# Kernel tuning notes

Hardware: AMD Instinct MI355X
Metric: run time of the kernel (lower is better)

## Reference

```python
import jax, jax.numpy as jnp
import numpy as np

N, E, B = 16000, 256000, 64
H = 4
DIMS = [960, 512, 256, 128]  # per-layer input dims; output dim of layer i is DIMS[i+1] = HID[i]*H
HID = [128, 64, 32]


def setup_inputs() -> dict:
    key = jax.random.key(0)
    ks = jax.random.split(key, 16)
    inp = {}
    inp["x"] = jax.random.normal(ks[0], (N, DIMS[0]), jnp.float32)
    inp["edge_index"] = jax.random.randint(ks[1], (2, E), 0, N)
    inp["batch"] = jnp.sort(jax.random.randint(ks[2], (N,), 0, B))
    k = 3
    for i in range(3):
        din, c = DIMS[i], HID[i]
        s = 1.0 / np.sqrt(din).astype(np.float32)
        inp[f"Wl{i+1}"] = jax.random.normal(ks[k], (din, H * c), jnp.float32) * s; k += 1
        inp[f"Wr{i+1}"] = jax.random.normal(ks[k], (din, H * c), jnp.float32) * s; k += 1
        inp[f"att{i+1}"] = jax.random.normal(ks[k], (H, c), jnp.float32) * (1.0 / np.sqrt(c).astype(np.float32)); k += 1
        inp[f"b{i+1}"] = jnp.zeros((H * c,), jnp.float32)
        inp[f"gnw{i+1}"] = jnp.ones((H * c,), jnp.float32)
        inp[f"gnb{i+1}"] = jnp.zeros((H * c,), jnp.float32)
        inp[f"gnm{i+1}"] = jnp.ones((H * c,), jnp.float32)
    d = DIMS[-1]
    inp["aW1"] = jax.random.normal(ks[k], (d, 128), jnp.float32) * (1.0 / np.sqrt(d).astype(np.float32)); k += 1
    inp["ab1"] = jnp.zeros((128,), jnp.float32)
    inp["aW2"] = jax.random.normal(ks[k], (128, 1), jnp.float32) * (1.0 / np.sqrt(128).astype(np.float32)); k += 1
    inp["ab2"] = jnp.zeros((1,), jnp.float32)
    return inp


def _gatv2(x, src, dst, Wl, Wr, att, bias):
    # PyG GATv2Conv, concat=True, negative_slope=0.2 (self-loops already in src/dst)
    n = x.shape[0]
    h, c = att.shape
    xl = (x @ Wl).reshape(n, h, c)
    xr = (x @ Wr).reshape(n, h, c)
    e = jax.nn.leaky_relu(xl[src] + xr[dst], negative_slope=0.2)  # [E,H,C]
    logit = jnp.einsum('ehc,hc->eh', e, att)                      # [E,H]
    m = jax.ops.segment_max(logit, dst, num_segments=n)
    m = jnp.nan_to_num(m, neginf=0.0)
    p = jnp.exp(logit - m[dst])
    z = jax.ops.segment_sum(p, dst, num_segments=n)
    alpha = p / (z[dst] + 1e-16)                                  # segment softmax over dst
    out = jax.ops.segment_sum(alpha[:, :, None] * xl[src], dst, num_segments=n)
    return out.reshape(n, h * c) + bias


def _graphnorm(x, w, b, ms, eps=1e-5):
    # PyG GraphNorm with batch=None: normalize over all nodes as one graph
    mean = jnp.mean(x, axis=0, keepdims=True)
    xc = x - ms * mean
    var = jnp.mean(xc * xc, axis=0, keepdims=True)
    return w * xc / jnp.sqrt(var + eps) + b


def reference(x, edge_index, batch,
              Wl1, Wr1, att1, b1, gnw1, gnb1, gnm1,
              Wl2, Wr2, att2, b2, gnw2, gnb2, gnm2,
              Wl3, Wr3, att3, b3, gnw3, gnb3, gnm3,
              aW1, ab1, aW2, ab2):
    n = x.shape[0]
    loop = jnp.arange(n)
    src = jnp.concatenate([edge_index[0], loop])  # add self-loops (PyG default)
    dst = jnp.concatenate([edge_index[1], loop])
    layers = [(Wl1, Wr1, att1, b1, gnw1, gnb1, gnm1),
              (Wl2, Wr2, att2, b2, gnw2, gnb2, gnm2),
              (Wl3, Wr3, att3, b3, gnw3, gnb3, gnm3)]
    for Wl, Wr, att, bb, gw, gb, gm in layers:
        x = _gatv2(x, src, dst, Wl, Wr, att, bb)
        x = _graphnorm(x, gw, gb, gm)
        x = jax.nn.relu(x)
    # AttentionalAggregation pooling: gate MLP -> segment softmax over graphs -> weighted sum
    gate = jax.nn.relu(x @ aW1 + ab1) @ aW2 + ab2  # [N,1]
    mg = jax.ops.segment_max(gate, batch, num_segments=B)
    mg = jnp.nan_to_num(mg, neginf=0.0)
    pg = jnp.exp(gate - mg[batch])
    zg = jax.ops.segment_sum(pg, batch, num_segments=B)
    a = pg / (zg[batch] + 1e-16)
    return jax.ops.segment_sum(a * x, batch, num_segments=B)  # [B, 128]
```

## Files before the change

kernel.cpp:

```cpp
#include <hip/hip_runtime.h>
#include <cstdint>
#include <cstddef>
#include <math.h>


typedef _Float16  h16x8  __attribute__((ext_vector_type(8)));
typedef _Float16  h16x4  __attribute__((ext_vector_type(4)));
typedef _Float16  h16x2  __attribute__((ext_vector_type(2)));
typedef float     f32x4  __attribute__((ext_vector_type(4)));

template<int R> struct HV;
template<> struct HV<8> { using T = h16x8; };
template<> struct HV<4> { using T = h16x4; };
template<> struct HV<2> { using T = h16x2; };

__device__ __forceinline__ void gload_lds16(const void* g, void* l) {
    __builtin_amdgcn_global_load_lds(
        (const __attribute__((address_space(1))) uint32_t*)g,
        (__attribute__((address_space(3))) uint32_t*)l, 16, 0, 0);
}

__device__ __forceinline__ int swz_k(int k, int row) {
    return (k & ~31) | ((((k >> 3) & 3) ^ ((row >> 1) & 3)) << 3) | (k & 7);
}

__device__ __forceinline__ void gn_coef(float s1, float s2, float w, float b,
                                        float ms, float invN, float& al, float& be) {
    float mean = s1 * invN;
    float ex2  = s2 * invN;
    float a    = ms * mean;
    float var  = ex2 - 2.f * a * mean + a * a;
    al = w * rsqrtf(var + 1e-5f);
    be = b - a * al;
}

__device__ __forceinline__ void conv_elem(int t, const float* __restrict__ Wl,
                                          const float* __restrict__ Wr,
                                          _Float16* __restrict__ Wt, int K, int HC) {
    int k = t / HC, n = t - k * HC;
    const int ks = swz_k(k, n);
    Wt[(size_t)n * K + ks] = (_Float16)Wl[t];
    if (Wr) Wt[(size_t)(HC + n) * K + ks] = (_Float16)Wr[t];
}

__global__ __launch_bounds__(256) void conv_all(
        const float* __restrict__ Wl0, const float* __restrict__ Wr0, _Float16* __restrict__ T0,
        const float* __restrict__ Wl1, const float* __restrict__ Wr1, _Float16* __restrict__ T1,
        const float* __restrict__ Wl2, const float* __restrict__ Wr2, _Float16* __restrict__ T2,
        const float* __restrict__ Wa, _Float16* __restrict__ Ta) {
    int t = blockIdx.x * blockDim.x + threadIdx.x;
    if (t < 491520) { conv_elem(t, Wl0, Wr0, T0, 960, 512); return; }
    t -= 491520;
    if (t < 131072) { conv_elem(t, Wl1, Wr1, T1, 512, 256); return; }
    t -= 131072;
    if (t < 32768)  { conv_elem(t, Wl2, Wr2, T2, 256, 128); return; }
    t -= 32768;
    if (t < 16384)  conv_elem(t, Wa, nullptr, Ta, 128, 128);
}

template<bool NORM>
__global__ __launch_bounds__(256) void prep_a(
        const float* __restrict__ X,
        const float* __restrict__ s1, const float* __restrict__ s2,
        const float* __restrict__ gw, const float* __restrict__ gb,
        const float* __restrict__ gm, float invN,
        _Float16* __restrict__ Out, int M, int K) {
    int t = blockIdx.x * blockDim.x + threadIdx.x;
    const int gpr = K >> 3;
    if (t >= M * gpr) return;
    int m = t / gpr, g = t - m * gpr;
    int k = g << 3;
    const float* src = X + (size_t)m * K + k;
    float4 u0 = *(const float4*)src;
    float4 u1 = *(const float4*)(src + 4);
    float uu[8] = {u0.x, u0.y, u0.z, u0.w, u1.x, u1.y, u1.z, u1.w};
    if (NORM) {
        #pragma unroll
        for (int j = 0; j < 8; ++j) {
            float al, be;
            gn_coef(s1[k + j], s2[k + j], gw[k + j], gb[k + j], gm[k + j],
                    invN, al, be);
            uu[j] = fmaxf(al * uu[j] + be, 0.f);
        }
    }
    h16x8 h;
    #pragma unroll
    for (int j = 0; j < 8; ++j) h[j] = (_Float16)uu[j];
    *(h16x8*)&Out[(size_t)m * K + swz_k(k, m)] = h;
}

template<bool BIAS, bool RELU, bool GATE, typename OutT>
__global__ __launch_bounds__(256) void mfma_gemm(
        const _Float16* __restrict__ A, const _Float16* __restrict__ Bt,
        const float* __restrict__ bias, OutT* __restrict__ C,
        OutT* __restrict__ C2, int CN,
        int M, int K, int N,
        const float* __restrict__ gw2, const float* __restrict__ gb2,
        float* __restrict__ gate) {
    __shared__ __attribute__((aligned(16))) _Float16 sA[2][128 * 32];
    __shared__ __attribute__((aligned(16))) _Float16 sB[2][128 * 32];
    __shared__ float gsum[128];

    const int gx  = gridDim.x;
    const int nwg = gx * gridDim.y;
    const int id  = blockIdx.y * gx + blockIdx.x;
    const int q   = nwg >> 3, r = nwg & 7;
    const int xcd = id & 7, sub = id >> 3;
    const int nid = (xcd < r) ? (xcd * (q + 1) + sub)
                              : (r * (q + 1) + (xcd - r) * q + sub);
    const int row0 = (nid / gx) * 128;
    const int col0 = (nid % gx) * 128;

    const int tid  = threadIdx.x;
    const int lane = tid & 63;
    const int w    = tid >> 6;
    const int wm   = w >> 1, wn = w & 1;
    const int lr   = lane & 15, lg = lane >> 4;
    const int bRow = w * 16 + (lane >> 2);
    const int bGrp = (lane & 3) * 8;
    const int fGrp = (lg ^ ((lr >> 1) & 3)) * 8;

    f32x4 acc[4][4] = {};

    const _Float16* pa = A  + (size_t)(row0 + bRow) * K + bGrp;
    const _Float16* pb = Bt + (size_t)(col0 + bRow) * K + bGrp;

    auto stage = [&](int buf, int k0) {
        gload_lds16(pa + k0,                  (char*)&sA[buf][0] + w * 1024);
        gload_lds16(pa + (size_t)64 * K + k0, (char*)&sA[buf][0] + 4096 + w * 1024);
        gload_lds16(pb + k0,                  (char*)&sB[buf][0] + w * 1024);
        gload_lds16(pb + (size_t)64 * K + k0, (char*)&sB[buf][0] + 4096 + w * 1024);
    };

    stage(0, 0);
    if (GATE) { if (tid < 128) gsum[tid] = 0.f; }
    __syncthreads();
    int cur = 0;
    for (int k0 = 0; k0 < K; k0 += 32) {
        if (k0 + 32 < K) stage(cur ^ 1, k0 + 32);
        h16x8 ah[4], bh[4];
        #pragma unroll
        for (int i = 0; i < 4; ++i) {
            ah[i] = *(const h16x8*)&sA[cur][(wm * 64 + i * 16 + lr) * 32 + fGrp];
            bh[i] = *(const h16x8*)&sB[cur][(wn * 64 + i * 16 + lr) * 32 + fGrp];
        }
        #pragma unroll
        for (int i = 0; i < 4; ++i)
            #pragma unroll
            for (int j = 0; j < 4; ++j)
                acc[i][j] = __builtin_amdgcn_mfma_f32_16x16x32_f16(ah[i], bh[j], acc[i][j], 0, 0, 0);
        __syncthreads();
        cur ^= 1;
    }

    if constexpr (!GATE) {
        OutT* co = (col0 < CN) ? C : C2;
        const int cb = (col0 < CN) ? col0 : col0 - CN;
        #pragma unroll
        for (int i = 0; i < 4; ++i) {
            const int rowb = row0 + wm * 64 + i * 16 + lg * 4;
            #pragma unroll
            for (int j = 0; j < 4; ++j) {
                const int col  = col0 + wn * 64 + j * 16 + lr;
                const int colw = cb   + wn * 64 + j * 16 + lr;
                const float bv = BIAS ? bias[col] : 0.f;
                #pragma unroll
                for (int qq = 0; qq < 4; ++qq) {
                    float v = acc[i][j][qq] + bv;
                    if (RELU) v = fmaxf(v, 0.f);
                    co[(size_t)(rowb + qq) * CN + colw] = (OutT)v;
                }
            }
        }
    } else {
        float gp[4][4] = {};
        float w2[4];
        #pragma unroll
        for (int j = 0; j < 4; ++j) w2[j] = gw2[wn * 64 + j * 16 + lr];
        #pragma unroll
        for (int i = 0; i < 4; ++i)
            #pragma unroll
            for (int j = 0; j < 4; ++j) {
                const int col = wn * 64 + j * 16 + lr;
                const float bv = bias[col];
                #pragma unroll
                for (int qq = 0; qq < 4; ++qq) {
                    float v = fmaxf(acc[i][j][qq] + bv, 0.f);
                    gp[i][qq] += v * w2[j];
                }
            }
        #pragma unroll
        for (int i = 0; i < 4; ++i)
            #pragma unroll
            for (int qq = 0; qq < 4; ++qq) {
                float pv = gp[i][qq];
                pv += __shfl_xor(pv, 1);
                pv += __shfl_xor(pv, 2);
                pv += __shfl_xor(pv, 4);
                pv += __shfl_xor(pv, 8);
                if (lr == 0) atomicAdd(&gsum[wm * 64 + i * 16 + lg * 4 + qq], pv);
            }
        __syncthreads();
        if (tid < 128) gate[row0 + tid] = gsum[tid] + gb2[0];
    }
}

__global__ void csr_count(const int* __restrict__ edst, int E, int Etot,
                          int* __restrict__ deg) {
    int e = blockIdx.x * blockDim.x + threadIdx.x;
    if (e >= Etot) return;
    int d = (e < E) ? edst[e] : e - E;
    atomicAdd(&deg[d], 1);
}

__global__ __launch_bounds__(1024) void scan_deg(const int* __restrict__ deg,
                                                 int* __restrict__ row_start,
                                                 int* __restrict__ cursor, int N) {
    __shared__ int part[1024];
    const int tid = threadIdx.x;
    const int base = tid * 16;
    int loc[16];
    int s = 0;
    #pragma unroll
    for (int j = 0; j < 16; ++j) {
        int i = base + j;
        s += (i < N) ? deg[i] : 0;
        loc[j] = s;
    }
    part[tid] = s; __syncthreads();
    #pragma unroll
    for (int off = 1; off < 1024; off <<= 1) {
        int t2 = (tid >= off) ? part[tid - off] : 0;
        __syncthreads();
        part[tid] += t2;
        __syncthreads();
    }
    const int pre = tid ? part[tid - 1] : 0;
    #pragma unroll
    for (int j = 0; j < 16; ++j) {
        int i = base + j;
        if (i < N) {
            int st = pre + (j ? loc[j - 1] : 0);
            row_start[i] = st;
            cursor[i]    = st;
            if (i == N - 1) row_start[N] = pre + loc[j];
        }
    }
}

__global__ void csr_fill(const int* __restrict__ esrc, const int* __restrict__ edst,
                         int E, int Etot, int* __restrict__ cursor,
                         int* __restrict__ src_perm) {
    int e = blockIdx.x * blockDim.x + threadIdx.x;
    if (e >= Etot) return;
    int s, d;
    if (e < E) { s = esrc[e]; d = edst[e]; }
    else       { s = d = e - E; }
    int pos = atomicAdd(&cursor[d], 1);
    src_perm[pos] = s;
}

template<int LOG2C>
__global__ __launch_bounds__(256) void gat_agg(
        const _Float16* __restrict__ xl, const _Float16* __restrict__ xr,
        const float* __restrict__ att, const float* __restrict__ bias,
        const int* __restrict__ row_start, const int* __restrict__ src_perm,
        int N, float* __restrict__ out) {
    constexpr int HC  = 4 << LOG2C;
    constexpr int R   = HC / 64;
    constexpr int P   = R / 2;
    constexpr int U   = 8;
    using hvec = typename HV<R>::T;

    const int widx = threadIdx.x >> 6;
    const int lane = threadIdx.x & 63;
    const int dst  = blockIdx.x * 4 + widx;
    if (dst >= N) return;

    const int base = lane * R;
    h16x2 xr2[P], at2[P];
    float acc[R];
    {
        hvec xv = *(const hvec*)&xr[(size_t)dst * HC + base];
        const h16x2* xp = (const h16x2*)&xv;
        #pragma unroll
        for (int i = 0; i < P; ++i) {
            xr2[i] = xp[i];
            h16x2 t;
            t[0] = (_Float16)att[base + 2 * i];
            t[1] = (_Float16)att[base + 2 * i + 1];
            at2[i] = t;
        }
        #pragma unroll
        for (int it = 0; it < R; ++it) acc[it] = 0.f;
    }
    h16x2 zp; zp[0] = (_Float16)0.f;  zp[1] = (_Float16)0.f;
    h16x2 sl; sl[0] = (_Float16)0.2f; sl[1] = (_Float16)0.2f;

    float z = 0.f;
    const int start = row_start[dst], end = row_start[dst + 1];

    auto do_edge = [&](const hvec& row) {
        const h16x2* r2 = (const h16x2*)&row;
        float a = 0.f;
        #pragma unroll
        for (int i = 0; i < P; ++i) {
            h16x2 s  = r2[i] + xr2[i];
            h16x2 lk = __builtin_elementwise_max(s, zp)
                     + __builtin_elementwise_min(s, zp) * sl;
            a = __builtin_amdgcn_fdot2(lk, at2[i], a, false);
        }
        #pragma unroll
        for (int sh = 1; sh < 16; sh <<= 1) a += __shfl_xor(a, sh);
        float p = __expf(a);
        z += p;
        #pragma unroll
        for (int it = 0; it < R; ++it) acc[it] += p * (float)row[it];
    };

    int cs = start;
    for (; cs + U <= end; cs += U) {
        hvec rows[U];
        #pragma unroll
        for (int k = 0; k < U; ++k) {
            int src = __builtin_amdgcn_readfirstlane(src_perm[cs + k]);
            rows[k] = *(const hvec*)&xl[(size_t)src * HC + base];
        }
        #pragma unroll
        for (int k = 0; k < U; ++k) do_edge(rows[k]);
    }
    for (; cs < end; ++cs) {
        int src = __builtin_amdgcn_readfirstlane(src_perm[cs]);
        hvec row = *(const hvec*)&xl[(size_t)src * HC + base];
        do_edge(row);
    }

    const float inv = 1.f / (z + 1e-16f);
    float ov[R];
    #pragma unroll
    for (int it = 0; it < R; ++it) ov[it] = acc[it] * inv + bias[base + it];
    float* po = out + (size_t)dst * HC + base;
    if constexpr (R == 8) {
        *(float4*)po       = make_float4(ov[0], ov[1], ov[2], ov[3]);
        *(float4*)(po + 4) = make_float4(ov[4], ov[5], ov[6], ov[7]);
    } else if constexpr (R == 4) {
        *(float4*)po = make_float4(ov[0], ov[1], ov[2], ov[3]);
    } else {
        *(float2*)po = make_float2(ov[0], ov[1]);
    }
}

__global__ __launch_bounds__(64) void colstats(const float* __restrict__ x, int HC,
                                               float* __restrict__ s1, float* __restrict__ s2) {
    int c  = blockIdx.x * 64 + threadIdx.x;
    int r0 = blockIdx.y * 128;
    float a = 0.f, b = 0.f;
    for (int r = r0; r < r0 + 128; ++r) {
        float v = x[(size_t)r * HC + c];
        a += v; b += v * v;
    }
    atomicAdd(&s1[c], a);
    atomicAdd(&s2[c], b);
}

__global__ __launch_bounds__(1024) void attn_pool(
        const float* __restrict__ x,
        const float* __restrict__ s1, const float* __restrict__ s2,
        const float* __restrict__ gw, const float* __restrict__ gb,
        const float* __restrict__ gm, float invN,
        const float* __restrict__ gate, const int* __restrict__ batch,
        int N, float* __restrict__ out) {
    const int b   = blockIdx.x;
    const int tid = threadIdx.x;
    const int grp = tid >> 7;
    const int ch  = tid & 127;
    int lo, hi;
    { int l = 0, r = N; while (l < r) { int mid = (l + r) >> 1; if (batch[mid] < b) l = mid + 1; else r = mid; } lo = l; }
    { int l = lo, r = N; while (l < r) { int mid = (l + r) >> 1; if (batch[mid] < b + 1) l = mid + 1; else r = mid; } hi = l; }
    if (lo >= hi) { if (tid < 128) out[b * 128 + tid] = 0.f; return; }

    float alc, bec;
    gn_coef(s1[ch], s2[ch], gw[ch], gb[ch], gm[ch], invN, alc, bec);

    __shared__ float red[1024];
    float mx = -INFINITY;
    for (int n = lo + tid; n < hi; n += 1024) mx = fmaxf(mx, gate[n]);
    red[tid] = mx; __syncthreads();
    for (int s = 512; s; s >>= 1) { if (tid < s) red[tid] = fmaxf(red[tid], red[tid + s]); __syncthreads(); }
    mx = red[0]; __syncthreads();
    float zs = 0.f;
    for (int n = lo + tid; n < hi; n += 1024) zs += __expf(gate[n] - mx);
    red[tid] = zs; __syncthreads();
    for (int s = 512; s; s >>= 1) { if (tid < s) red[tid] += red[tid + s]; __syncthreads(); }
    zs = red[0]; __syncthreads();
    float acc = 0.f;
    for (int n = lo + grp; n < hi; n += 8) {
        float wv = __expf(gate[n] - mx);
        float v  = fmaxf(alc * x[(size_t)n * 128 + ch] + bec, 0.f);
        acc += wv * v;
    }
    red[tid] = acc; __syncthreads();
    if (tid < 128) {
        float s = red[tid];
        #pragma unroll
        for (int g = 1; g < 8; ++g) s += red[g * 128 + tid];
        out[b * 128 + tid] = s / (zs + 1e-16f);
    }
}

extern "C" void kernel_launch(void* const* d_in, const int* in_sizes, int n_in,
                              void* d_out, int out_size, void* d_ws, size_t ws_size,
                              hipStream_t stream) {
    const float* x0  = (const float*)d_in[0];
    const int* edge  = (const int*)d_in[1];
    const int* batch = (const int*)d_in[2];
    const int N = in_sizes[2];
    const int E = in_sizes[1] / 2;
    const int Etot = E + N;
    const int dims[4] = {960, 512, 256, 128};

    const float* Wl[3]   = {(const float*)d_in[3],  (const float*)d_in[10], (const float*)d_in[17]};
    const float* Wr[3]   = {(const float*)d_in[4],  (const float*)d_in[11], (const float*)d_in[18]};
    const float* attp[3] = {(const float*)d_in[5],  (const float*)d_in[12], (const float*)d_in[19]};
    const float* bi[3]   = {(const float*)d_in[6],  (const float*)d_in[13], (const float*)d_in[20]};
    const float* gw[3]   = {(const float*)d_in[7],  (const float*)d_in[14], (const float*)d_in[21]};
    const float* gb[3]   = {(const float*)d_in[8],  (const float*)d_in[15], (const float*)d_in[22]};
    const float* gm[3]   = {(const float*)d_in[9],  (const float*)d_in[16], (const float*)d_in[23]};
    const float* aW1 = (const float*)d_in[24];
    const float* ab1 = (const float*)d_in[25];
    const float* aW2 = (const float*)d_in[26];
    const float* ab2 = (const float*)d_in[27];

    size_t off = 0;
    auto alloc = [&](size_t bytes) -> char* {
        char* p = (char*)d_ws + off;
        off += (bytes + 255) & ~(size_t)255;
        return p;
    };
    _Float16* xlB     = (_Float16*)alloc((size_t)N * 512 * 2);
    _Float16* xrB     = (_Float16*)alloc((size_t)N * 512 * 2);
    _Float16* aT      = (_Float16*)alloc((size_t)N * 960 * 2);
    float*   bufC     = (float*)alloc((size_t)N * 512 * 4);
    int*     deg      = (int*)alloc((size_t)N * 4);
    int*     row_start= (int*)alloc((size_t)(N + 1) * 4);
    int*     cursor   = (int*)alloc((size_t)N * 4);
    int*     src_perm = (int*)alloc((size_t)Etot * 4);
    float*   s12      = (float*)alloc(3 * 1024 * 4);
    float*   gateB    = (float*)alloc((size_t)N * 4);
    _Float16* wt[3];
    for (int l = 0; l < 3; ++l)
        wt[l] = (_Float16*)alloc((size_t)dims[l] * (2 * dims[l + 1]) * 2);
    _Float16* awt = (_Float16*)alloc(128 * 128 * 2);
    (void)ws_size; (void)n_in; (void)out_size;

    const float invN = 1.0f / N;

    conv_all<<<(671744 + 255) / 256, 256, 0, stream>>>(
        Wl[0], Wr[0], wt[0], Wl[1], Wr[1], wt[1], Wl[2], Wr[2], wt[2], aW1, awt);

    hipMemsetAsync(deg, 0, (size_t)N * sizeof(int), stream);
    hipMemsetAsync(s12, 0, 3 * 1024 * sizeof(float), stream);
    csr_count<<<(Etot + 255) / 256, 256, 0, stream>>>(edge + E, E, Etot, deg);
    scan_deg<<<1, 1024, 0, stream>>>(deg, row_start, cursor, N);
    csr_fill<<<(Etot + 255) / 256, 256, 0, stream>>>(edge, edge + E, E, Etot,
                                                     cursor, src_perm);

    for (int l = 0; l < 3; ++l) {
        const int K = dims[l], HC = dims[l + 1];
        const int ngrp = N * (K >> 3);
        if (l == 0)
            prep_a<false><<<(ngrp + 255) / 256, 256, 0, stream>>>(
                x0, nullptr, nullptr, nullptr, nullptr, nullptr, 0.f, aT, N, K);
        else
            prep_a<true><<<(ngrp + 255) / 256, 256, 0, stream>>>(
                bufC, s12 + (l - 1) * 1024, s12 + (l - 1) * 1024 + 512,
                gw[l - 1], gb[l - 1], gm[l - 1], invN, aT, N, K);

        dim3 ggrid((2 * HC) / 128, N / 128);
        mfma_gemm<false, false, false, _Float16><<<ggrid, 256, 0, stream>>>(
            aT, wt[l], nullptr, xlB, xrB, HC, N, K, 2 * HC,
            nullptr, nullptr, nullptr);

        const int agrid = (N + 3) / 4;
        if (l == 0)      gat_agg<7><<<agrid, 256, 0, stream>>>(xlB, xrB, attp[l], bi[l], row_start, src_perm, N, bufC);
        else if (l == 1) gat_agg<6><<<agrid, 256, 0, stream>>>(xlB, xrB, attp[l], bi[l], row_start, src_perm, N, bufC);
        else             gat_agg<5><<<agrid, 256, 0, stream>>>(xlB, xrB, attp[l], bi[l], row_start, src_perm, N, bufC);

        colstats<<<dim3(HC / 64, N / 128), 64, 0, stream>>>(bufC, HC, s12 + l * 1024, s12 + l * 1024 + 512);
    }

    prep_a<true><<<(N * 16 + 255) / 256, 256, 0, stream>>>(
        bufC, s12 + 2048, s12 + 2048 + 512, gw[2], gb[2], gm[2], invN, aT, N, 128);
    mfma_gemm<true, true, true, float><<<dim3(1, N / 128), 256, 0, stream>>>(
        aT, awt, ab1, nullptr, nullptr, 128, N, 128, 128, aW2, ab2, gateB);
    attn_pool<<<64, 1024, 0, stream>>>(bufC, s12 + 2048, s12 + 2048 + 512,
                                       gw[2], gb[2], gm[2], invN, gateB, batch, N, (float*)d_out);
}
```

Before: 325.2 us.

## Store aggregation output in fp16 and restructure GEMM to 2 waves per block

The intermediate GAT aggregation buffer changes from fp32 to fp16, halving its traffic in gat_agg writes, colstats, prep_a and attn_pool reads. The MFMA GEMM moves from 4 waves in a 2x2 layout to 2 waves, each computing a 64x128 tile, which raises per-wave register use and B-fragment reuse. The gate epilogue now writes directly without the shared-memory atomic reduction. The two memsets are merged into one by placing s12 right after deg. The fp16 intermediate adds rounding error to the normalisation statistics, and the smaller workgroups may change occupancy.

```diff
diff --git a/kernel.cpp b/kernel.cpp
--- a/kernel.cpp
+++ b/kernel.cpp
@@ -58,9 +58,9 @@
     if (t < 16384)  conv_elem(t, Wa, nullptr, Ta, 128, 128);
 }
 
-template<bool NORM>
+template<typename InT, bool NORM>
 __global__ __launch_bounds__(256) void prep_a(
-        const float* __restrict__ X,
+        const InT* __restrict__ X,
         const float* __restrict__ s1, const float* __restrict__ s2,
         const float* __restrict__ gw, const float* __restrict__ gb,
         const float* __restrict__ gm, float invN,
@@ -70,10 +70,18 @@
     if (t >= M * gpr) return;
     int m = t / gpr, g = t - m * gpr;
     int k = g << 3;
-    const float* src = X + (size_t)m * K + k;
-    float4 u0 = *(const float4*)src;
-    float4 u1 = *(const float4*)(src + 4);
-    float uu[8] = {u0.x, u0.y, u0.z, u0.w, u1.x, u1.y, u1.z, u1.w};
+    float uu[8];
+    if constexpr (sizeof(InT) == 4) {
+        const float* src = (const float*)X + (size_t)m * K + k;
+        float4 u0 = *(const float4*)src;
+        float4 u1 = *(const float4*)(src + 4);
+        uu[0] = u0.x; uu[1] = u0.y; uu[2] = u0.z; uu[3] = u0.w;
+        uu[4] = u1.x; uu[5] = u1.y; uu[6] = u1.z; uu[7] = u1.w;
+    } else {
+        h16x8 hv = *(const h16x8*)((const _Float16*)X + (size_t)m * K + k);
+        #pragma unroll
+        for (int j = 0; j < 8; ++j) uu[j] = (float)hv[j];
+    }
     if (NORM) {
         #pragma unroll
         for (int j = 0; j < 8; ++j) {
@@ -90,7 +98,7 @@
 }
 
 template<bool BIAS, bool RELU, bool GATE, typename OutT>
-__global__ __launch_bounds__(256) void mfma_gemm(
+__global__ __launch_bounds__(128) void mfma_gemm(
         const _Float16* __restrict__ A, const _Float16* __restrict__ Bt,
         const float* __restrict__ bias, OutT* __restrict__ C,
         OutT* __restrict__ C2, int CN,
@@ -99,7 +107,6 @@
         float* __restrict__ gate) {
     __shared__ __attribute__((aligned(16))) _Float16 sA[2][128 * 32];
     __shared__ __attribute__((aligned(16))) _Float16 sB[2][128 * 32];
-    __shared__ float gsum[128];
 
     const int gx  = gridDim.x;
     const int nwg = gx * gridDim.y;
@@ -114,40 +121,42 @@
     const int tid  = threadIdx.x;
     const int lane = tid & 63;
     const int w    = tid >> 6;
-    const int wm   = w >> 1, wn = w & 1;
     const int lr   = lane & 15, lg = lane >> 4;
-    const int bRow = w * 16 + (lane >> 2);
-    const int bGrp = (lane & 3) * 8;
+    const int sRow = lane >> 2;
+    const int sGrp = (lane & 3) * 8;
     const int fGrp = (lg ^ ((lr >> 1) & 3)) * 8;
 
-    f32x4 acc[4][4] = {};
-
-    const _Float16* pa = A  + (size_t)(row0 + bRow) * K + bGrp;
-    const _Float16* pb = Bt + (size_t)(col0 + bRow) * K + bGrp;
+    f32x4 acc[4][8] = {};
+
+    const _Float16* pa = A  + (size_t)(row0 + w * 64 + sRow) * K + sGrp;
+    const _Float16* pb = Bt + (size_t)(col0 + w * 64 + sRow) * K + sGrp;
 
     auto stage = [&](int buf, int k0) {
-        gload_lds16(pa + k0,                  (char*)&sA[buf][0] + w * 1024);
-        gload_lds16(pa + (size_t)64 * K + k0, (char*)&sA[buf][0] + 4096 + w * 1024);
-        gload_lds16(pb + k0,                  (char*)&sB[buf][0] + w * 1024);
-        gload_lds16(pb + (size_t)64 * K + k0, (char*)&sB[buf][0] + 4096 + w * 1024);
+        #pragma unroll
+        for (int j = 0; j < 4; ++j) {
+            gload_lds16(pa + (size_t)(j * 16) * K + k0,
+                        (char*)&sA[buf][0] + w * 4096 + j * 1024);
+            gload_lds16(pb + (size_t)(j * 16) * K + k0,
+                        (char*)&sB[buf][0] + w * 4096 + j * 1024);
+        }
     };
 
     stage(0, 0);
-    if (GATE) { if (tid < 128) gsum[tid] = 0.f; }
     __syncthreads();
     int cur = 0;
     for (int k0 = 0; k0 < K; k0 += 32) {
         if (k0 + 32 < K) stage(cur ^ 1, k0 + 32);
-        h16x8 ah[4], bh[4];
-        #pragma unroll
-        for (int i = 0; i < 4; ++i) {
-            ah[i] = *(const h16x8*)&sA[cur][(wm * 64 + i * 16 + lr) * 32 + fGrp];
-            bh[i] = *(const h16x8*)&sB[cur][(wn * 64 + i * 16 + lr) * 32 + fGrp];
-        }
+        h16x8 ah[4], bh[8];
+        #pragma unroll
+        for (int i = 0; i < 4; ++i)
+            ah[i] = *(const h16x8*)&sA[cur][(w * 64 + i * 16 + lr) * 32 + fGrp];
+        #pragma unroll
+        for (int j = 0; j < 8; ++j)
+            bh[j] = *(const h16x8*)&sB[cur][(j * 16 + lr) * 32 + fGrp];
         #pragma unroll
         for (int i = 0; i < 4; ++i)
             #pragma unroll
-            for (int j = 0; j < 4; ++j)
+            for (int j = 0; j < 8; ++j)
                 acc[i][j] = __builtin_amdgcn_mfma_f32_16x16x32_f16(ah[i], bh[j], acc[i][j], 0, 0, 0);
         __syncthreads();
         cur ^= 1;
@@ -158,11 +167,11 @@
         const int cb = (col0 < CN) ? col0 : col0 - CN;
         #pragma unroll
         for (int i = 0; i < 4; ++i) {
-            const int rowb = row0 + wm * 64 + i * 16 + lg * 4;
+            const int rowb = row0 + w * 64 + i * 16 + lg * 4;
             #pragma unroll
-            for (int j = 0; j < 4; ++j) {
-                const int col  = col0 + wn * 64 + j * 16 + lr;
-                const int colw = cb   + wn * 64 + j * 16 + lr;
+            for (int j = 0; j < 8; ++j) {
+                const int col  = col0 + j * 16 + lr;
+                const int colw = cb   + j * 16 + lr;
                 const float bv = BIAS ? bias[col] : 0.f;
                 #pragma unroll
                 for (int qq = 0; qq < 4; ++qq) {
@@ -174,15 +183,14 @@
         }
     } else {
         float gp[4][4] = {};
-        float w2[4];
-        #pragma unroll
-        for (int j = 0; j < 4; ++j) w2[j] = gw2[wn * 64 + j * 16 + lr];
+        float w2[8];
+        #pragma unroll
+        for (int j = 0; j < 8; ++j) w2[j] = gw2[j * 16 + lr];
         #pragma unroll
         for (int i = 0; i < 4; ++i)
             #pragma unroll
-            for (int j = 0; j < 4; ++j) {
-                const int col = wn * 64 + j * 16 + lr;
-                const float bv = bias[col];
+            for (int j = 0; j < 8; ++j) {
+                const float bv = bias[j * 16 + lr];
                 #pragma unroll
                 for (int qq = 0; qq < 4; ++qq) {
                     float v = fmaxf(acc[i][j][qq] + bv, 0.f);
@@ -198,10 +206,9 @@
                 pv += __shfl_xor(pv, 2);
                 pv += __shfl_xor(pv, 4);
                 pv += __shfl_xor(pv, 8);
-                if (lr == 0) atomicAdd(&gsum[wm * 64 + i * 16 + lg * 4 + qq], pv);
+                if (lr == 0)
+                    gate[row0 + w * 64 + i * 16 + lg * 4 + qq] = pv + gb2[0];
             }
-        __syncthreads();
-        if (tid < 128) gate[row0 + tid] = gsum[tid] + gb2[0];
     }
 }
 
@@ -265,7 +272,7 @@
         const _Float16* __restrict__ xl, const _Float16* __restrict__ xr,
         const float* __restrict__ att, const float* __restrict__ bias,
         const int* __restrict__ row_start, const int* __restrict__ src_perm,
-        int N, float* __restrict__ out) {
+        int N, _Float16* __restrict__ out) {
     constexpr int HC  = 4 << LOG2C;
     constexpr int R   = HC / 64;
     constexpr int P   = R / 2;
@@ -336,27 +343,20 @@
     }
 
     const float inv = 1.f / (z + 1e-16f);
-    float ov[R];
+    hvec ov;
     #pragma unroll
-    for (int it = 0; it < R; ++it) ov[it] = acc[it] * inv + bias[base + it];
-    float* po = out + (size_t)dst * HC + base;
-    if constexpr (R == 8) {
-        *(float4*)po       = make_float4(ov[0], ov[1], ov[2], ov[3]);
-        *(float4*)(po + 4) = make_float4(ov[4], ov[5], ov[6], ov[7]);
-    } else if constexpr (R == 4) {
-        *(float4*)po = make_float4(ov[0], ov[1], ov[2], ov[3]);
-    } else {
-        *(float2*)po = make_float2(ov[0], ov[1]);
-    }
-}
-
-__global__ __launch_bounds__(64) void colstats(const float* __restrict__ x, int HC,
+    for (int it = 0; it < R; ++it)
+        ov[it] = (_Float16)(acc[it] * inv + bias[base + it]);
+    *(hvec*)&out[(size_t)dst * HC + base] = ov;
+}
+
+__global__ __launch_bounds__(64) void colstats(const _Float16* __restrict__ x, int HC,
                                                float* __restrict__ s1, float* __restrict__ s2) {
     int c  = blockIdx.x * 64 + threadIdx.x;
     int r0 = blockIdx.y * 128;
     float a = 0.f, b = 0.f;
     for (int r = r0; r < r0 + 128; ++r) {
-        float v = x[(size_t)r * HC + c];
+        float v = (float)x[(size_t)r * HC + c];
         a += v; b += v * v;
     }
     atomicAdd(&s1[c], a);
@@ -364,7 +364,7 @@
 }
 
 __global__ __launch_bounds__(1024) void attn_pool(
-        const float* __restrict__ x,
+        const _Float16* __restrict__ x,
         const float* __restrict__ s1, const float* __restrict__ s2,
         const float* __restrict__ gw, const float* __restrict__ gb,
         const float* __restrict__ gm, float invN,
@@ -396,7 +396,7 @@
     float acc = 0.f;
     for (int n = lo + grp; n < hi; n += 8) {
         float wv = __expf(gate[n] - mx);
-        float v  = fmaxf(alc * x[(size_t)n * 128 + ch] + bec, 0.f);
+        float v  = fmaxf(alc * (float)x[(size_t)n * 128 + ch] + bec, 0.f);
         acc += wv * v;
     }
     red[tid] = acc; __syncthreads();
@@ -440,12 +440,12 @@
     _Float16* xlB     = (_Float16*)alloc((size_t)N * 512 * 2);
     _Float16* xrB     = (_Float16*)alloc((size_t)N * 512 * 2);
     _Float16* aT      = (_Float16*)alloc((size_t)N * 960 * 2);
-    float*   bufC     = (float*)alloc((size_t)N * 512 * 4);
+    _Float16* bufC    = (_Float16*)alloc((size_t)N * 512 * 2);
     int*     deg      = (int*)alloc((size_t)N * 4);
+    float*   s12      = (float*)alloc(3 * 1024 * 4);
     int*     row_start= (int*)alloc((size_t)(N + 1) * 4);
     int*     cursor   = (int*)alloc((size_t)N * 4);
     int*     src_perm = (int*)alloc((size_t)Etot * 4);
-    float*   s12      = (float*)alloc(3 * 1024 * 4);
     float*   gateB    = (float*)alloc((size_t)N * 4);
     _Float16* wt[3];
     for (int l = 0; l < 3; ++l)
@@ -458,8 +458,7 @@
     conv_all<<<(671744 + 255) / 256, 256, 0, stream>>>(
         Wl[0], Wr[0], wt[0], Wl[1], Wr[1], wt[1], Wl[2], Wr[2], wt[2], aW1, awt);
 
-    hipMemsetAsync(deg, 0, (size_t)N * sizeof(int), stream);
-    hipMemsetAsync(s12, 0, 3 * 1024 * sizeof(float), stream);
+    hipMemsetAsync(deg, 0, (size_t)N * 4 + 3 * 1024 * 4, stream);
     csr_count<<<(Etot + 255) / 256, 256, 0, stream>>>(edge + E, E, Etot, deg);
     scan_deg<<<1, 1024, 0, stream>>>(deg, row_start, cursor, N);
     csr_fill<<<(Etot + 255) / 256, 256, 0, stream>>>(edge, edge + E, E, Etot,
@@ -469,15 +468,15 @@
         const int K = dims[l], HC = dims[l + 1];
         const int ngrp = N * (K >> 3);
         if (l == 0)
-            prep_a<false><<<(ngrp + 255) / 256, 256, 0, stream>>>(
+            prep_a<float, false><<<(ngrp + 255) / 256, 256, 0, stream>>>(
                 x0, nullptr, nullptr, nullptr, nullptr, nullptr, 0.f, aT, N, K);
         else
-            prep_a<true><<<(ngrp + 255) / 256, 256, 0, stream>>>(
+            prep_a<_Float16, true><<<(ngrp + 255) / 256, 256, 0, stream>>>(
                 bufC, s12 + (l - 1) * 1024, s12 + (l - 1) * 1024 + 512,
                 gw[l - 1], gb[l - 1], gm[l - 1], invN, aT, N, K);
 
         dim3 ggrid((2 * HC) / 128, N / 128);
-        mfma_gemm<false, false, false, _Float16><<<ggrid, 256, 0, stream>>>(
+        mfma_gemm<false, false, false, _Float16><<<ggrid, 128, 0, stream>>>(
             aT, wt[l], nullptr, xlB, xrB, HC, N, K, 2 * HC,
             nullptr, nullptr, nullptr);
 
@@ -489,9 +488,9 @@
         colstats<<<dim3(HC / 64, N / 128), 64, 0, stream>>>(bufC, HC, s12 + l * 1024, s12 + l * 1024 + 512);
     }
 
-    prep_a<true><<<(N * 16 + 255) / 256, 256, 0, stream>>>(
+    prep_a<_Float16, true><<<(N * 16 + 255) / 256, 256, 0, stream>>>(
         bufC, s12 + 2048, s12 + 2048 + 512, gw[2], gb[2], gm[2], invN, aT, N, 128);
-    mfma_gemm<true, true, true, float><<<dim3(1, N / 128), 256, 0, stream>>>(
+    mfma_gemm<true, true, true, float><<<dim3(1, N / 128), 128, 0, stream>>>(
         aT, awt, ab1, nullptr, nullptr, 128, N, 128, 128, aW2, ab2, gateB);
     attn_pool<<<64, 1024, 0, stream>>>(bufC, s12 + 2048, s12 + 2048 + 512,
                                        gw[2], gb[2], gm[2], invN, gateB, batch, N, (float*)d_out);
```

Result: slower. 338.5 us (+4.1%).
